# Optimization experiments

Hardware: AMD Instinct MI355X
Metric: run time of the kernel (lower is better)

The kernel has to match this reference:

```python
import jax, jax.numpy as jnp
import numpy as np
from jax import lax

C_IN, C_OUT, K = 32, 64, 3
SUPPORT_LEN, ORDER = 1, 2
GC_IN = (ORDER * SUPPORT_LEN + 1) * C_IN  # 96
N, V, T = 32, 500, 96


def _conv2d_1xk(x, w, b):
    # x: (N,C,V,T), w: (O,I,1,K), valid padding -> (N,O,V,T-K+1)
    y = lax.conv_general_dilated(x, w, window_strides=(1, 1), padding='VALID',
                                 dimension_numbers=('NCHW', 'OIHW', 'NCHW'))
    return y + b[None, :, None, None]


def setup_inputs() -> dict:
    key = jax.random.key(0)
    ks = jax.random.split(key, 12)
    x = jax.random.normal(ks[0], (N, C_IN, V, T), dtype=jnp.float32)
    A = jax.random.uniform(ks[1], (V, V), dtype=jnp.float32)
    A = A / jnp.sum(A, axis=1, keepdims=True)  # random-walk normalization
    s = 1.0 / np.sqrt(C_IN * K)
    w1 = jax.random.uniform(ks[2], (C_IN, C_IN, 1, K), jnp.float32, -s, s)
    b1 = jax.random.uniform(ks[3], (C_IN,), jnp.float32, -s, s)
    w2 = jax.random.uniform(ks[4], (C_IN, C_IN, 1, K), jnp.float32, -s, s)
    b2 = jax.random.uniform(ks[5], (C_IN,), jnp.float32, -s, s)
    w3 = jax.random.uniform(ks[6], (C_IN, C_IN, 1, K), jnp.float32, -s, s)
    b3 = jax.random.uniform(ks[7], (C_IN,), jnp.float32, -s, s)
    so = 1.0 / np.sqrt(GC_IN)
    w_out = jax.random.uniform(ks[8], (C_OUT, GC_IN), jnp.float32, -so, so)
    b_out = jax.random.uniform(ks[9], (C_OUT,), jnp.float32, -so, so)
    prelu_a = jnp.asarray(0.25, dtype=jnp.float32)
    return {"x": x, "A": A, "w1": w1, "b1": b1, "w2": w2, "b2": b2,
            "w3": w3, "b3": b3, "w_out": w_out, "b_out": b_out,
            "prelu_a": prelu_a}


def reference(x, A, w1, b1, w2, b2, w3, b3, w_out, b_out, prelu_a):
    # TimeBlock: gated temporal conv with residual-relu
    temp = _conv2d_1xk(x, w1, b1) + jax.nn.sigmoid(_conv2d_1xk(x, w2, b2))
    xt = jax.nn.relu(temp + _conv2d_1xk(x, w3, b3))  # (N,C,V,T-2)
    # gcn: multi-hop diffusion, order=2, single support
    x1 = jnp.einsum('ncvl,vw->ncwl', xt, A)
    x2 = jnp.einsum('ncvl,vw->ncwl', x1, A)
    h = jnp.concatenate([xt, x1, x2], axis=1)  # (N,3C,V,T-2)
    # 1x1 conv projection
    out = jnp.einsum('ncvl,oc->novl', h, w_out) + b_out[None, :, None, None]
    # PReLU (scalar parameter); dropout is a no-op (training=self.training, eval)
    out = jnp.where(out > 0, out, prelu_a * out)
    return out
```

## Files before the change

kernel.cpp:

```cpp
#include <hip/hip_runtime.h>
#include <stdint.h>


typedef float  f32x4  __attribute__((ext_vector_type(4)));
typedef float  f32x2  __attribute__((ext_vector_type(2)));
typedef short  bf16x8 __attribute__((ext_vector_type(8)));

static __device__ __forceinline__ unsigned short f2bf(float f) {
    union { float f; unsigned u; } v; v.f = f;
    unsigned u = v.u;
    return (unsigned short)((u + 0x7fffu + ((u >> 16) & 1u)) >> 16);
}

#define WS_S   ((size_t)1024 * 64 * 96 * 8 * 2)
#define AT_B   (512u * 512u * 2u)
#define WA_B   (3u * 96u * 32u * 2u)

static __device__ __forceinline__ int swz(int row, int q) {
    return q ^ (row & 3) ^ ((row >> 2) & 3);
}

__global__ __launch_bounds__(256)
void prep_kernel(const float* __restrict__ A,
                 const float* __restrict__ w1, const float* __restrict__ w2,
                 const float* __restrict__ w3, const float* __restrict__ wout,
                 unsigned short* __restrict__ At, unsigned short* __restrict__ Wa,
                 unsigned short* __restrict__ Wo)
{
    int idx = blockIdx.x * 256 + threadIdx.x;
    if (idx < 512 * 512) {
        int w = idx >> 9, v = idx & 511;
        float val = (w < 500 && v < 500) ? A[v * 500 + w] : 0.f;
        At[idx] = f2bf(val);
    } else if (idx < 512 * 512 + 3 * 3 * 32 * 32) {
        int t = idx - 512 * 512;
        int ci = t & 31;
        int co = (t >> 5) & 31;
        int rc = t >> 10;
        int conv = rc % 3, koff = rc / 3;
        const float* ws = (conv == 0) ? w1 : ((conv == 1) ? w2 : w3);
        Wa[t] = f2bf(ws[co * 96 + ci * 3 + koff]);
    } else if (idx < 512 * 512 + 3 * 3 * 32 * 32 + 64 * 96) {
        int t = idx - (512 * 512 + 3 * 3 * 32 * 32);
        Wo[t] = f2bf(wout[t]);
    }
}

__global__ __launch_bounds__(512, 1)
void conv_kernel(const float* __restrict__ x, const unsigned short* __restrict__ Wa,
                 const float* __restrict__ b1, const float* __restrict__ b2,
                 const float* __restrict__ b3, unsigned short* __restrict__ xt)
{
    __shared__ unsigned short Xs2[52 * 256];
    __shared__ unsigned short WaSh[9216];
    __shared__ unsigned short stash[32 * 408];

    const int th   = blockIdx.x;
    const int vblk = blockIdx.y;
    const int n    = blockIdx.z;
    const int tid  = threadIdx.x;
    const int lane = tid & 63, wv = tid >> 6;
    const int cl = lane & 15, q4 = lane >> 4;
    const int nbase = wv * 48;

    for (int g = tid; g < 1152; g += 512)
        *(uint4*)&WaSh[g * 8] = *(const uint4*)(Wa + g * 8);

    for (int s = 0; s < 2; ++s) {
        int fid = tid + s * 512;
        if (fid < 832) {
            int rq = fid / 13, seg = fid % 13;
            int vv = rq & 7, i4 = rq >> 3;
            int v = vblk * 8 + vv;
            int tbase = th * 48 + seg * 4;
            float b[4][4];
            #pragma unroll
            for (int di = 0; di < 4; ++di) {
                float4 f = make_float4(0.f, 0.f, 0.f, 0.f);
                if (v < 500 && tbase < 96)
                    f = *(const float4*)(x + (((size_t)n * 32 + i4 * 4 + di) * 500 + v) * 96 + tbase);
                b[di][0] = f.x; b[di][1] = f.y; b[di][2] = f.z; b[di][3] = f.w;
            }
            #pragma unroll
            for (int j = 0; j < 4; ++j) {
                uint2 u;
                u.x = (unsigned)f2bf(b[0][j]) | ((unsigned)f2bf(b[1][j]) << 16);
                u.y = (unsigned)f2bf(b[2][j]) | ((unsigned)f2bf(b[3][j]) << 16);
                *(uint2*)&Xs2[(seg * 4 + j) * 256 + vv * 32 + i4 * 4] = u;
            }
        }
    }

    float bb1[2][4], bb2[2][4], bb3[2][4];
    #pragma unroll
    for (int p = 0; p < 2; ++p)
        #pragma unroll
        for (int r = 0; r < 4; ++r) {
            int c = p * 16 + q4 * 4 + r;
            bb1[p][r] = b1[c]; bb2[p][r] = b2[c]; bb3[p][r] = b3[c];
        }

    __syncthreads();

    bf16x8 af[6][3];
    #pragma unroll
    for (int mt = 0; mt < 6; ++mt)
        #pragma unroll
        for (int ko = 0; ko < 3; ++ko)
            af[mt][ko] = *(const bf16x8*)&WaSh[ko * 3072 + (mt * 16 + cl) * 32 + q4 * 8];

    f32x4 acc[6][3];
    #pragma unroll
    for (int mt = 0; mt < 6; ++mt)
        #pragma unroll
        for (int nt = 0; nt < 3; ++nt)
            acc[mt][nt] = (f32x4){0.f, 0.f, 0.f, 0.f};

    #pragma unroll
    for (int ko = 0; ko < 3; ++ko) {
        #pragma unroll
        for (int nt = 0; nt < 3; ++nt) {
            int col = nbase + nt * 16 + cl;
            int ll = col >> 3, vv = col & 7;
            bf16x8 bf = *(const bf16x8*)&Xs2[(ll + ko) * 256 + vv * 32 + q4 * 8];
            #pragma unroll
            for (int mt = 0; mt < 6; ++mt)
                acc[mt][nt] = __builtin_amdgcn_mfma_f32_16x16x32_bf16(
                    af[mt][ko], bf, acc[mt][nt], 0, 0, 0);
        }
    }

    #pragma unroll
    for (int p = 0; p < 2; ++p) {
        #pragma unroll
        for (int nt = 0; nt < 3; ++nt) {
            int col = nbase + nt * 16 + cl;
            int ll = col >> 3, vv = col & 7;
            bool valid = (th * 48 + ll) < 94;
            #pragma unroll
            for (int r = 0; r < 4; ++r) {
                float a0 = acc[p][nt][r];
                float a1 = acc[2 + p][nt][r];
                float a2 = acc[4 + p][nt][r];
                float sg = 1.f / (1.f + __expf(-(a1 + bb2[p][r])));
                float o  = fmaxf(a0 + bb1[p][r] + sg + a2 + bb3[p][r], 0.f);
                int c = p * 16 + q4 * 4 + r;
                stash[c * 408 + ll * 8 + vv] = valid ? f2bf(o) : (unsigned short)0;
            }
        }
    }
    __syncthreads();

    for (int g = tid; g < 1536; g += 512) {
        int c = g / 48, sg = g % 48;
        uint4 val = *(const uint4*)&stash[c * 408 + sg * 8];
        *(uint4*)(xt + ((((size_t)n * 32 + c) * 64 + vblk) * 96 + th * 48) * 8 + sg * 8) = val;
    }
}

__global__ __launch_bounds__(256)
void hop_kernel(const unsigned short* __restrict__ At,
                const unsigned short* __restrict__ src,
                unsigned short* __restrict__ dst)
{
    __shared__ unsigned short Ash[128 * 4 * 8];
    __shared__ unsigned short Bsh[96 * 4 * 8];

    const int bid = blockIdx.x;
    const int xcd = bid & 7;
    const int s = bid >> 3;
    const int mtile = s & 3;
    const int b = xcd * 128 + (s >> 2);
    const int tid = threadIdx.x;
    const int lane = tid & 63, wv = tid >> 6;
    const int mhalf = (wv & 1) * 64, nhalf = (wv >> 1) * 48;
    const int col = lane & 15, q4 = lane >> 4;

    f32x4 acc[4][3];
    #pragma unroll
    for (int mt = 0; mt < 4; ++mt)
        #pragma unroll
        for (int nt = 0; nt < 3; ++nt)
            acc[mt][nt] = (f32x4){0.f, 0.f, 0.f, 0.f};

    const unsigned short* Abase = At + (size_t)(mtile * 128) * 512;
    const unsigned short* Bbase = src + (size_t)b * 64 * 96 * 8;

    for (int kc = 0; kc < 16; ++kc) {
        __syncthreads();
        #pragma unroll
        for (int t2 = 0; t2 < 2; ++t2) {
            int idx = tid + t2 * 256;
            int r = idx >> 2, q = idx & 3;
            uint4 val = *(const uint4*)(Abase + (size_t)r * 512 + kc * 32 + q * 8);
            *(uint4*)&Ash[(r * 4 + swz(r, q)) * 8] = val;
        }
        for (int g = tid; g < 384; g += 256) {
            int q = g / 96, l = g % 96;
            uint4 val = *(const uint4*)(Bbase + ((size_t)(kc * 4 + q) * 96 + l) * 8);
            *(uint4*)&Bsh[(l * 4 + swz(l, q)) * 8] = val;
        }
        __syncthreads();

        bf16x8 af[4], bfr[3];
        #pragma unroll
        for (int mt = 0; mt < 4; ++mt) {
            int r = mhalf + mt * 16 + col;
            af[mt] = *(const bf16x8*)&Ash[(r * 4 + swz(r, q4)) * 8];
        }
        #pragma unroll
        for (int nt = 0; nt < 3; ++nt) {
            int l = nhalf + nt * 16 + col;
            bfr[nt] = *(const bf16x8*)&Bsh[(l * 4 + swz(l, q4)) * 8];
        }
        #pragma unroll
        for (int mt = 0; mt < 4; ++mt)
            #pragma unroll
            for (int nt = 0; nt < 3; ++nt)
                acc[mt][nt] = __builtin_amdgcn_mfma_f32_16x16x32_bf16(
                    af[mt], bfr[nt], acc[mt][nt], 0, 0, 0);
    }

    #pragma unroll
    for (int mt = 0; mt < 4; ++mt) {
        int w0 = mtile * 128 + mhalf + mt * 16 + q4 * 4;
        int vblk = w0 >> 3, vv0 = w0 & 7;
        #pragma unroll
        for (int nt = 0; nt < 3; ++nt) {
            int l = nhalf + nt * 16 + col;
            uint2 u;
            u.x = (unsigned)f2bf(acc[mt][nt].x) | ((unsigned)f2bf(acc[mt][nt].y) << 16);
            u.y = (unsigned)f2bf(acc[mt][nt].z) | ((unsigned)f2bf(acc[mt][nt].w) << 16);
            *(uint2*)(dst + (((size_t)b * 64 + vblk) * 96 + l) * 8 + vv0) = u;
        }
    }
}

__global__ __launch_bounds__(512, 1)
void proj_kernel(const unsigned short* __restrict__ Wo,
                 const unsigned short* __restrict__ xt,
                 const unsigned short* __restrict__ x1,
                 const unsigned short* __restrict__ x2,
                 const float* __restrict__ bout,
                 const float* __restrict__ prelu_a,
                 float* __restrict__ out)
{
    __shared__ unsigned short WoSh[64 * 12 * 8];
    __shared__ unsigned short Bsh[768 * 4 * 8];

    const int vblk = blockIdx.x;
    const int n = blockIdx.y;
    const int tid = threadIdx.x;
    const int lane = tid & 63, wv = tid >> 6;
    const int colL = lane & 15, q4 = lane >> 4;

    for (int g = tid; g < 768; g += 512) {
        int o = g / 12, slot = g % 12;
        int kc = slot >> 2, qq = slot & 3;
        uint4 val = *(const uint4*)(Wo + o * 96 + slot * 8);
        *(uint4*)&WoSh[(o * 12 + kc * 4 + swz(o, qq)) * 8] = val;
    }

    f32x4 acc[4][6];
    #pragma unroll
    for (int mt = 0; mt < 4; ++mt)
        #pragma unroll
        for (int nt = 0; nt < 6; ++nt)
            acc[mt][nt] = (f32x4){0.f, 0.f, 0.f, 0.f};

    const unsigned short* planes[3] = {xt, x1, x2};
    for (int kc = 0; kc < 3; ++kc) {
        __syncthreads();
        const unsigned short* P = planes[kc];
        #pragma unroll
        for (int s = 0; s < 6; ++s) {
            int idx = tid + s * 512;
            int cl = idx / 96, l = idx % 96;
            union { uint4 u; unsigned short sh[8]; } val;
            val.u = *(const uint4*)(P + (((size_t)(n * 32 + cl)) * 64 + vblk) * 96 * 8
                                      + (size_t)l * 8);
            int cq = cl >> 3, cw = cl & 7;
            #pragma unroll
            for (int vv = 0; vv < 8; ++vv) {
                int colv = vv * 96 + l;
                Bsh[(colv * 4 + swz(colv, cq)) * 8 + cw] = val.sh[vv];
            }
        }
        __syncthreads();

        bf16x8 af[4], bfr[6];
        #pragma unroll
        for (int mt = 0; mt < 4; ++mt) {
            int o = mt * 16 + colL;
            af[mt] = *(const bf16x8*)&WoSh[(o * 12 + kc * 4 + swz(o, q4)) * 8];
        }
        #pragma unroll
        for (int nt = 0; nt < 6; ++nt) {
            int colv = wv * 96 + nt * 16 + colL;
            bfr[nt] = *(const bf16x8*)&Bsh[(colv * 4 + swz(colv, q4)) * 8];
        }
        #pragma unroll
        for (int mt = 0; mt < 4; ++mt)
            #pragma unroll
            for (int nt = 0; nt < 6; ++nt)
                acc[mt][nt] = __builtin_amdgcn_mfma_f32_16x16x32_bf16(
                    af[mt], bfr[nt], acc[mt][nt], 0, 0, 0);
    }

    const float pa = prelu_a[0];
    const int v = vblk * 8 + wv;
    if (v < 500) {
        #pragma unroll
        for (int mt = 0; mt < 4; ++mt) {
            #pragma unroll
            for (int r = 0; r < 4; ++r) {
                int o = mt * 16 + q4 * 4 + r;
                float bo = bout[o];
                float* orow = out + (((size_t)n * 64 + o) * 500 + v) * 94;
                #pragma unroll
                for (int nt = 0; nt < 6; ++nt) {
                    int l = nt * 16 + colL;
                    if (l < 94) {
                        float val = acc[mt][nt][r] + bo;
                        val = (val > 0.f) ? val : pa * val;
                        orow[l] = val;
                    }
                }
            }
        }
    }
}

extern "C" void kernel_launch(void* const* d_in, const int* in_sizes, int n_in,
                              void* d_out, int out_size, void* d_ws, size_t ws_size,
                              hipStream_t stream)
{
    const float* x    = (const float*)d_in[0];
    const float* A    = (const float*)d_in[1];
    const float* w1   = (const float*)d_in[2];
    const float* b1   = (const float*)d_in[3];
    const float* w2   = (const float*)d_in[4];
    const float* b2   = (const float*)d_in[5];
    const float* w3   = (const float*)d_in[6];
    const float* b3   = (const float*)d_in[7];
    const float* wout = (const float*)d_in[8];
    const float* bout = (const float*)d_in[9];
    const float* pa   = (const float*)d_in[10];
    float* out = (float*)d_out;

    char* ws = (char*)d_ws;
    unsigned short* xt = (unsigned short*)(ws);
    unsigned short* x1 = (unsigned short*)(ws + WS_S);
    unsigned short* x2 = (unsigned short*)(ws + 2 * WS_S);
    unsigned short* At = (unsigned short*)(ws + 3 * WS_S);
    unsigned short* Wa = (unsigned short*)(ws + 3 * WS_S + AT_B);
    unsigned short* Wo = (unsigned short*)(ws + 3 * WS_S + AT_B + WA_B);

    const int prep_elems = 512 * 512 + 3 * 3 * 32 * 32 + 64 * 96;
    prep_kernel<<<dim3((prep_elems + 255) / 256), 256, 0, stream>>>(
        A, w1, w2, w3, wout, At, Wa, Wo);
    conv_kernel<<<dim3(2, 63, 32), 512, 0, stream>>>(x, Wa, b1, b2, b3, xt);
    hop_kernel<<<dim3(4096), 256, 0, stream>>>(At, xt, x1);
    hop_kernel<<<dim3(4096), 256, 0, stream>>>(At, x1, x2);
    proj_kernel<<<dim3(63, 32), 512, 0, stream>>>(Wo, xt, x1, x2, bout, pa, out);
}
```

Baseline: 922.9 us.

## Pre-swizzle A into MFMA fragment layout and process two batches per hop block

The prep kernel now writes the transposed adjacency matrix directly in per-lane MFMA fragment order, so hop_kernel loads A fragments straight from global memory into registers and no longer stages A in shared memory. Each hop block now handles two (n,c) batch slices with K chunks of 64, using an 8-way swizzle for B, and each wave computes a 64x96 tile. This halves the grid, reuses each A fragment load across twice as many output columns, and halves the barrier count. In exchange it uses more accumulator registers (24 f32x4) and relies on the A fragment loads being cached.

Result: faster. 840.3 us (-9.0%).

```diff
diff --git a/kernel.cpp b/kernel.cpp
--- a/kernel.cpp
+++ b/kernel.cpp
@@ -18,6 +18,9 @@
 
 static __device__ __forceinline__ int swz(int row, int q) {
     return q ^ (row & 3) ^ ((row >> 2) & 3);
+}
+static __device__ __forceinline__ int swz8(int row, int q) {
+    return q ^ (row & 7);
 }
 
 __global__ __launch_bounds__(256)
@@ -29,7 +32,14 @@
 {
     int idx = blockIdx.x * 256 + threadIdx.x;
     if (idx < 512 * 512) {
-        int w = idx >> 9, v = idx & 511;
+        int t = idx;
+        int e   = t & 7;
+        int col = (t >> 3) & 15;
+        int q4  = (t >> 7) & 3;
+        int kc  = (t >> 9) & 15;
+        int rg  = t >> 13;
+        int w = rg * 16 + col;
+        int v = kc * 32 + q4 * 8 + e;
         float val = (w < 500 && v < 500) ? A[v * 500 + w] : 0.f;
         At[idx] = f2bf(val);
     } else if (idx < 512 * 512 + 3 * 3 * 32 * 32) {
@@ -159,79 +169,83 @@
 }
 
 __global__ __launch_bounds__(256)
-void hop_kernel(const unsigned short* __restrict__ At,
+void hop_kernel(const unsigned short* __restrict__ At_fr,
                 const unsigned short* __restrict__ src,
                 unsigned short* __restrict__ dst)
 {
-    __shared__ unsigned short Ash[128 * 4 * 8];
-    __shared__ unsigned short Bsh[96 * 4 * 8];
+    __shared__ unsigned short Bsh[2 * 96 * 8 * 8];
 
     const int bid = blockIdx.x;
     const int xcd = bid & 7;
     const int s = bid >> 3;
     const int mtile = s & 3;
-    const int b = xcd * 128 + (s >> 2);
+    const int bp = xcd * 64 + (s >> 2);
+    const int b0 = bp * 2;
     const int tid = threadIdx.x;
     const int lane = tid & 63, wv = tid >> 6;
-    const int mhalf = (wv & 1) * 64, nhalf = (wv >> 1) * 48;
+    const int mhalf = (wv & 1) * 64;
+    const int bsel = wv >> 1;
     const int col = lane & 15, q4 = lane >> 4;
 
-    f32x4 acc[4][3];
+    f32x4 acc[4][6];
     #pragma unroll
     for (int mt = 0; mt < 4; ++mt)
         #pragma unroll
-        for (int nt = 0; nt < 3; ++nt)
+        for (int nt = 0; nt < 6; ++nt)
             acc[mt][nt] = (f32x4){0.f, 0.f, 0.f, 0.f};
 
-    const unsigned short* Abase = At + (size_t)(mtile * 128) * 512;
-    const unsigned short* Bbase = src + (size_t)b * 64 * 96 * 8;
-
-    for (int kc = 0; kc < 16; ++kc) {
+    const unsigned short* Bbase = src + (size_t)b0 * 64 * 96 * 8;
+
+    for (int kc2 = 0; kc2 < 8; ++kc2) {
+        bf16x8 af[4][2];
+        #pragma unroll
+        for (int mt = 0; mt < 4; ++mt) {
+            int rg = mtile * 8 + (wv & 1) * 4 + mt;
+            #pragma unroll
+            for (int sub = 0; sub < 2; ++sub) {
+                int kc = kc2 * 2 + sub;
+                af[mt][sub] = *(const bf16x8*)(At_fr + ((size_t)(rg * 16 + kc) * 512) + lane * 8);
+            }
+        }
+
         __syncthreads();
         #pragma unroll
-        for (int t2 = 0; t2 < 2; ++t2) {
-            int idx = tid + t2 * 256;
-            int r = idx >> 2, q = idx & 3;
-            uint4 val = *(const uint4*)(Abase + (size_t)r * 512 + kc * 32 + q * 8);
-            *(uint4*)&Ash[(r * 4 + swz(r, q)) * 8] = val;
-        }
-        for (int g = tid; g < 384; g += 256) {
-            int q = g / 96, l = g % 96;
-            uint4 val = *(const uint4*)(Bbase + ((size_t)(kc * 4 + q) * 96 + l) * 8);
-            *(uint4*)&Bsh[(l * 4 + swz(l, q)) * 8] = val;
+        for (int i = 0; i < 6; ++i) {
+            int g = tid + i * 256;
+            int bs = g / 768;
+            int rem = g % 768;
+            int q = rem / 96, l = rem % 96;
+            uint4 val = *(const uint4*)(Bbase + (((size_t)bs * 64 + kc2 * 8 + q) * 96 + l) * 8);
+            *(uint4*)&Bsh[(((bs * 96 + l) * 8) + swz8(l, q)) * 8] = val;
         }
         __syncthreads();
 
-        bf16x8 af[4], bfr[3];
-        #pragma unroll
-        for (int mt = 0; mt < 4; ++mt) {
-            int r = mhalf + mt * 16 + col;
-            af[mt] = *(const bf16x8*)&Ash[(r * 4 + swz(r, q4)) * 8];
-        }
-        #pragma unroll
-        for (int nt = 0; nt < 3; ++nt) {
-            int l = nhalf + nt * 16 + col;
-            bfr[nt] = *(const bf16x8*)&Bsh[(l * 4 + swz(l, q4)) * 8];
-        }
-        #pragma unroll
-        for (int mt = 0; mt < 4; ++mt)
-            #pragma unroll
-            for (int nt = 0; nt < 3; ++nt)
-                acc[mt][nt] = __builtin_amdgcn_mfma_f32_16x16x32_bf16(
-                    af[mt], bfr[nt], acc[mt][nt], 0, 0, 0);
-    }
-
+        #pragma unroll
+        for (int sub = 0; sub < 2; ++sub) {
+            #pragma unroll
+            for (int nt = 0; nt < 6; ++nt) {
+                int l = nt * 16 + col;
+                bf16x8 bfr = *(const bf16x8*)&Bsh[(((bsel * 96 + l) * 8) + swz8(l, sub * 4 + q4)) * 8];
+                #pragma unroll
+                for (int mt = 0; mt < 4; ++mt)
+                    acc[mt][nt] = __builtin_amdgcn_mfma_f32_16x16x32_bf16(
+                        af[mt][sub], bfr, acc[mt][nt], 0, 0, 0);
+            }
+        }
+    }
+
+    const size_t b = b0 + bsel;
     #pragma unroll
     for (int mt = 0; mt < 4; ++mt) {
         int w0 = mtile * 128 + mhalf + mt * 16 + q4 * 4;
         int vblk = w0 >> 3, vv0 = w0 & 7;
         #pragma unroll
-        for (int nt = 0; nt < 3; ++nt) {
-            int l = nhalf + nt * 16 + col;
+        for (int nt = 0; nt < 6; ++nt) {
+            int l = nt * 16 + col;
             uint2 u;
             u.x = (unsigned)f2bf(acc[mt][nt].x) | ((unsigned)f2bf(acc[mt][nt].y) << 16);
             u.y = (unsigned)f2bf(acc[mt][nt].z) | ((unsigned)f2bf(acc[mt][nt].w) << 16);
-            *(uint2*)(dst + (((size_t)b * 64 + vblk) * 96 + l) * 8 + vv0) = u;
+            *(uint2*)(dst + ((b * 64 + vblk) * 96 + l) * 8 + vv0) = u;
         }
     }
 }
@@ -360,7 +374,7 @@
     prep_kernel<<<dim3((prep_elems + 255) / 256), 256, 0, stream>>>(
         A, w1, w2, w3, wout, At, Wa, Wo);
     conv_kernel<<<dim3(2, 63, 32), 512, 0, stream>>>(x, Wa, b1, b2, b3, xt);
-    hop_kernel<<<dim3(4096), 256, 0, stream>>>(At, xt, x1);
-    hop_kernel<<<dim3(4096), 256, 0, stream>>>(At, x1, x2);
+    hop_kernel<<<dim3(2048), 256, 0, stream>>>(At, xt, x1);
+    hop_kernel<<<dim3(2048), 256, 0, stream>>>(At, x1, x2);
     proj_kernel<<<dim3(63, 32), 512, 0, stream>>>(Wo, xt, x1, x2, bout, pa, out);
 }
```
